# Kernel tuning notes

Hardware: AMD Instinct MI355X
Metric: run time of the kernel (lower is better)

## Reference

```python
import jax, jax.numpy as jnp
import numpy as np

N = 25000      # nodes per type
E = 300000     # weight-edge rows
K = 16         # neighbors
F = 64         # in_feat
A = 64         # atten_dim
DW = 64        # weight_dim
CB = 8         # num_bit_conv
CV = 8         # num_vector_conv
OUT = 64       # out_feat
IN_K = CB * F + CV * (3 + 2 + 1)


def setup_inputs() -> dict:
    key = jax.random.key(0)
    ks = jax.random.split(key, 40)
    s = 0.05
    d = {}
    d['eu'] = jax.random.normal(ks[0], (N, F), jnp.float32)
    d['ei'] = jax.random.normal(ks[1], (N, F), jnp.float32)
    d['et'] = jax.random.normal(ks[2], (N, F), jnp.float32)
    d['ew'] = jax.random.normal(ks[3], (E, DW), jnp.float32)
    names = ['u_iw_j', 'u_tw_j', 'i_uw_j', 'i_tw_j', 't_uw_j', 't_iw_j']
    for i, nm in enumerate(names):
        d[nm] = jax.random.randint(ks[4 + i], (N, K), 0, N, jnp.int64 if jax.config.jax_enable_x64 else jnp.int32)
        d[nm.replace('_j', '_w')] = jax.random.randint(ks[10 + i], (N, K), 0, E, jnp.int64 if jax.config.jax_enable_x64 else jnp.int32)
    # per-type Attention1 params: user, item, tag
    for i, t in enumerate(['user', 'item', 'tag']):
        b = 16 + 4 * i
        d[f'W1_{t}'] = jax.random.normal(ks[b], (F + DW, A), jnp.float32) * s
        d[f'W2_{t}'] = jax.random.normal(ks[b + 1], (F, A), jnp.float32) * s
        d[f'b_{t}'] = jax.random.normal(ks[b + 2], (1, A), jnp.float32) * s
        d[f'v_{t}'] = jax.random.normal(ks[b + 3], (1, A), jnp.float32) * s
    d['U'] = jax.random.normal(ks[28], (F, A), jnp.float32) * s
    d['q'] = jax.random.normal(ks[29], (1, A), jnp.float32) * s
    d['p'] = jax.random.normal(ks[30], (1, A), jnp.float32) * s
    d['W_bit'] = jax.random.normal(ks[31], (CB, 3), jnp.float32) * s       # Conv2d(1,CB,(3,1))
    d['W_vec1'] = jax.random.normal(ks[32], (CV, 1, F), jnp.float32) * s   # Conv2d(1,CV,(1,F))
    d['W_vec2'] = jax.random.normal(ks[33], (CV, 2, F), jnp.float32) * s
    d['W_vec3'] = jax.random.normal(ks[34], (CV, 3, F), jnp.float32) * s
    d['Wf'] = jax.random.normal(ks[35], (IN_K, OUT), jnp.float32) * s
    d['bf'] = jax.random.normal(ks[36], (1, OUT), jnp.float32) * s
    return d


def _atten1(ev, ej, ew, v_j, v_w, W1, W2, b, v):
    ejp = jnp.concatenate([jnp.zeros((1, ej.shape[1]), ej.dtype), ej], axis=0)
    ewp = jnp.concatenate([jnp.zeros((1, ew.shape[1]), ew.dtype), ew], axis=0)
    eNj = ejp[v_j]                                  # [N,K,F]
    eNw = ewp[v_w]                                  # [N,K,DW]
    eNv = jnp.broadcast_to(ev[:, None, :], (ev.shape[0], v_j.shape[1], ev.shape[1]))
    eN_vw = jnp.concatenate([eNv, eNw], axis=-1)    # [N,K,F+DW]
    av = jnp.einsum('nkd,da->nka', eN_vw, W1) + jnp.einsum('nkf,fa->nka', eNj, W2) + b
    x = jax.nn.relu(av) @ v.T                       # [N,K,1]
    a = jax.nn.softmax(x, axis=1)
    return jnp.sum(a * eNj, axis=1)                 # [N,F]


def _atten2(u, i, t, U, q, p):
    uit = jnp.stack([u, i, t], axis=1)              # [N,3,F]
    x = jnp.einsum('nsf,fa->nsa', uit, U) + q
    x = jax.nn.relu(x) @ p.T                        # [N,3,1]
    b = jax.nn.softmax(x, axis=1)
    return b * uit                                  # [N,3,F]


def _conv(eN, W_bit, W_vec1, W_vec2, W_vec3):
    # eN: [N,3,F]
    bit = jax.nn.relu(jnp.einsum('njf,cj->ncf', eN, W_bit))       # [N,CB,F]
    bit = bit.reshape(bit.shape[0], -1)
    vec = []
    for j, W in ((1, W_vec1), (2, W_vec2), (3, W_vec3)):
        win = jnp.stack([eN[:, s:s + j, :] for s in range(3 - j + 1)], axis=1)  # [N,4-j,j,F]
        y = jax.nn.relu(jnp.einsum('nsjf,cjf->ncs', win, W))       # [N,CV,4-j]
        vec.append(y.reshape(y.shape[0], -1))
    return jnp.concatenate([bit] + vec, axis=1)                    # [N,IN_K]


def _forward(eu, ei, et, ew, params, idx):
    (W1u, W2u, bu, vu, W1i, W2i, bi, vi, W1t, W2t, bt, vt,
     U, q, p, W_bit, W_vec1, W_vec2, W_vec3, Wf, bf) = params
    (u_iw_j, u_iw_w, u_tw_j, u_tw_w, i_uw_j, i_uw_w,
     i_tw_j, i_tw_w, t_uw_j, t_uw_w, t_iw_j, t_iw_w) = idx
    eu_iN = _atten1(eu, ei, ew, u_iw_j, u_iw_w, W1i, W2i, bi, vi)
    eu_tN = _atten1(eu, et, ew, u_tw_j, u_tw_w, W1t, W2t, bt, vt)
    ei_uN = _atten1(ei, eu, ew, i_uw_j, i_uw_w, W1u, W2u, bu, vu)
    ei_tN = _atten1(ei, et, ew, i_tw_j, i_tw_w, W1t, W2t, bt, vt)
    et_uN = _atten1(et, eu, ew, t_uw_j, t_uw_w, W1u, W2u, bu, vu)
    et_iN = _atten1(et, ei, ew, t_iw_j, t_iw_w, W1i, W2i, bi, vi)
    euN = _atten2(eu, eu_iN, eu_tN, U, q, p)
    eiN = _atten2(ei_uN, ei, ei_tN, U, q, p)
    etN = _atten2(et_uN, et_iN, et, U, q, p)
    out = []
    for eN in (euN, eiN, etN):
        c = _conv(eN, W_bit, W_vec1, W_vec2, W_vec3)
        out.append(jax.nn.relu(c @ Wf + bf))
    return tuple(out)


def reference(eu, ei, et, ew,
              u_iw_j, u_iw_w, u_tw_j, u_tw_w, i_uw_j, i_uw_w, i_tw_j, i_tw_w,
              t_uw_j, t_uw_w, t_iw_j, t_iw_w,
              W1_user, W2_user, b_user, v_user,
              W1_item, W2_item, b_item, v_item,
              W1_tag, W2_tag, b_tag, v_tag,
              U, q, p, W_bit, W_vec1, W_vec2, W_vec3, Wf, bf):
    params = (W1_user, W2_user, b_user, v_user, W1_item, W2_item, b_item, v_item,
              W1_tag, W2_tag, b_tag, v_tag, U, q, p, W_bit, W_vec1, W_vec2, W_vec3, Wf, bf)
    idx = (u_iw_j, u_iw_w, u_tw_j, u_tw_w, i_uw_j, i_uw_w,
           i_tw_j, i_tw_w, t_uw_j, t_uw_w, t_iw_j, t_iw_w)
    return _forward(eu, ei, et, ew, params, idx)
```

## Files before the change

kernel.cpp:

```cpp
#include <hip/hip_runtime.h>
#include <math.h>

#define NN 25000
#define EE 300000
#define NT 1563
#define NT64 391
#define ET64 4688

typedef __attribute__((ext_vector_type(8))) short bf16x8;
typedef __attribute__((ext_vector_type(4))) float f32x4;
typedef __attribute__((ext_vector_type(2))) float f32x2;
typedef __attribute__((ext_vector_type(2))) __fp16 h2;

__device__ __forceinline__ unsigned short f2bf(float f) {
    union { float f; unsigned u; } a; a.f = f;
    unsigned r = (a.u + 0x7fffu + ((a.u >> 16) & 1u)) >> 16;
    return (unsigned short)r;
}
__device__ __forceinline__ unsigned pack2(float lo, float hi) {
    return (unsigned)f2bf(lo) | ((unsigned)f2bf(hi) << 16);
}
__device__ __forceinline__ float bflo(unsigned p) {
    union { unsigned u; float f; } a; a.u = p << 16; return a.f;
}
__device__ __forceinline__ float bfhi(unsigned p) {
    union { unsigned u; float f; } a; a.u = p & 0xffff0000u; return a.f;
}
__device__ __forceinline__ unsigned packfp8x4(float a, float b, float c, float d) {
    int v = __builtin_amdgcn_cvt_pk_fp8_f32(a, b, 0, 0);
    v = __builtin_amdgcn_cvt_pk_fp8_f32(c, d, v, 1);
    return (unsigned)v;
}
__device__ __forceinline__ unsigned pkh(float lo, float hi) {
    h2 r = __builtin_amdgcn_cvt_pkrtz(lo, hi);
    return __builtin_bit_cast(unsigned, r);
}
template<bool HI>
__device__ __forceinline__ h2 fp8toh(unsigned v) {
#if __has_builtin(__builtin_amdgcn_cvt_scalef32_pk_f16_fp8)
    return __builtin_amdgcn_cvt_scalef32_pk_f16_fp8((int)v, 1.0f, HI);
#else
    f32x2 f = __builtin_amdgcn_cvt_pk_f32_fp8((int)v, HI);
    return __builtin_amdgcn_cvt_pkrtz(f.x, f.y);
#endif
}
__device__ __forceinline__ float hdot(h2 a, h2 b, float c) {
#if __has_builtin(__builtin_amdgcn_fdot2)
    return __builtin_amdgcn_fdot2(a, b, c, false);
#else
    return c + (float)a[0] * (float)b[0] + (float)a[1] * (float)b[1];
#endif
}
__device__ __forceinline__ h2 hmax0(h2 a) {
    h2 z; z[0] = (__fp16)0.f; z[1] = (__fp16)0.f;
#if __has_builtin(__builtin_elementwise_max)
    return __builtin_elementwise_max(a, z);
#else
    h2 r;
    r[0] = a[0] > z[0] ? a[0] : z[0];
    r[1] = a[1] > z[1] ? a[1] : z[1];
    return r;
#endif
}

__global__ __launch_bounds__(256) void head_kernel(
    const float* __restrict__ ew,
    const float* __restrict__ eu, const float* __restrict__ ei, const float* __restrict__ et,
    const float* __restrict__ W1u, const float* __restrict__ W1i, const float* __restrict__ W1t,
    const float* __restrict__ W2u, const float* __restrict__ W2i, const float* __restrict__ W2t,
    const float* __restrict__ bu, const float* __restrict__ bi, const float* __restrict__ bt,
    unsigned char* __restrict__ gw8, unsigned* __restrict__ preB,
    unsigned char* __restrict__ JG)
{
    __shared__ __align__(16) unsigned short stA[64 * 72];
    __shared__ __align__(16) float cS[64 * 68];
    const int t = threadIdx.x;
    const int lane = t & 63, wv = t >> 6;
    const int l15 = lane & 15, quad = lane >> 4;
    const int cw = wv * 16 + l15;
    const int bx = blockIdx.x;

    if (bx < ET64) {
        if (bx == 0 && t < 48) {
            int w = t >> 4;
            ((unsigned*)(gw8 + (size_t)w * (EE + 1) * 64))[t & 15] = 0u;
        }
        const float* Ws[3] = { W1u + 4096, W1i + 4096, W1t + 4096 };
        bf16x8 bf[3][2];
        #pragma unroll
        for (int w = 0; w < 3; ++w)
            #pragma unroll
            for (int ks = 0; ks < 2; ++ks)
                #pragma unroll
                for (int j = 0; j < 8; ++j)
                    bf[w][ks][j] = (short)f2bf(Ws[w][(ks * 32 + quad * 8 + j) * 64 + cw]);

        const int rowBase = bx * 64;
        #pragma unroll
        for (int i = 0; i < 4; ++i) {
            int idx = t + i * 256;
            int row = idx >> 4, cg = idx & 15;
            int gr = rowBase + row;
            float4 v4 = (gr < EE) ? *(const float4*)(ew + (size_t)gr * 64 + cg * 4)
                                  : make_float4(0.f, 0.f, 0.f, 0.f);
            uint2 pk = { pack2(v4.x, v4.y), pack2(v4.z, v4.w) };
            *(uint2*)&stA[row * 72 + cg * 4] = pk;
        }
        __syncthreads();
        bf16x8 af[4][2];
        #pragma unroll
        for (int m = 0; m < 4; ++m)
            #pragma unroll
            for (int ks = 0; ks < 2; ++ks)
                af[m][ks] = *(const bf16x8*)&stA[(m * 16 + l15) * 72 + ks * 32 + quad * 8];

        #pragma unroll
        for (int w = 0; w < 3; ++w) {
            if (w) __syncthreads();
            f32x4 acc[4];
            #pragma unroll
            for (int m = 0; m < 4; ++m) {
                acc[m].x = 0; acc[m].y = 0; acc[m].z = 0; acc[m].w = 0;
                #pragma unroll
                for (int ks = 0; ks < 2; ++ks)
                    acc[m] = __builtin_amdgcn_mfma_f32_16x16x32_bf16(af[m][ks], bf[w][ks], acc[m], 0, 0, 0);
                #pragma unroll
                for (int r = 0; r < 4; ++r)
                    cS[(m * 16 + quad * 4 + r) * 68 + cw] = acc[m][r];
            }
            __syncthreads();
            unsigned char* outg = gw8 + (size_t)w * (EE + 1) * 64 + 64;
            #pragma unroll
            for (int i = 0; i < 2; ++i) {
                int task = t + i * 256;
                int row = task >> 3, seg = task & 7;
                int gr = rowBase + row;
                if (gr < EE) {
                    float4 a = *(const float4*)&cS[row * 68 + seg * 8];
                    float4 b = *(const float4*)&cS[row * 68 + seg * 8 + 4];
                    uint2 pk = { packfp8x4(a.x, a.y, a.z, a.w),
                                 packfp8x4(b.x, b.y, b.z, b.w) };
                    *(uint2*)(outg + (size_t)gr * 64 + seg * 8) = pk;
                }
            }
        }
    } else {
        const int yy = bx - ET64;
        const int y = yy / NT64;
        const int rowBase = (yy - y * NT64) * 64;
        if (rowBase == 0 && t < 48)
            ((unsigned*)(JG + (size_t)y * (NN + 1) * 192))[t] = 0u;
        const float* X; const float* Wa; const float* Wb; const float* W2;
        const float* ba; const float* bb; int oa, ob;
        switch (y) {
            case 0:  X = eu; Wa = W1i; ba = bi; oa = 0; Wb = W1t; bb = bt; ob = 1; W2 = W2u; break;
            case 1:  X = ei; Wa = W1u; ba = bu; oa = 2; Wb = W1t; bb = bt; ob = 3; W2 = W2i; break;
            default: X = et; Wa = W1u; ba = bu; oa = 4; Wb = W1i; bb = bi; ob = 5; W2 = W2t; break;
        }
        const float* Ws[3] = { Wa, Wb, W2 };
        const float bias_cw[3] = { ba[cw], bb[cw], 0.f };
        bf16x8 bf[3][2];
        #pragma unroll
        for (int w = 0; w < 3; ++w)
            #pragma unroll
            for (int ks = 0; ks < 2; ++ks)
                #pragma unroll
                for (int j = 0; j < 8; ++j)
                    bf[w][ks][j] = (short)f2bf(Ws[w][(ks * 32 + quad * 8 + j) * 64 + cw]);

        #pragma unroll
        for (int i = 0; i < 4; ++i) {
            int idx = t + i * 256;
            int row = idx >> 4, cg = idx & 15;
            int gr = rowBase + row;
            float4 v4 = (gr < NN) ? *(const float4*)(X + (size_t)gr * 64 + cg * 4)
                                  : make_float4(0.f, 0.f, 0.f, 0.f);
            uint2 pk = { pack2(v4.x, v4.y), pack2(v4.z, v4.w) };
            *(uint2*)&stA[row * 72 + cg * 4] = pk;
        }
        __syncthreads();
        bf16x8 af[4][2];
        #pragma unroll
        for (int m = 0; m < 4; ++m)
            #pragma unroll
            for (int ks = 0; ks < 2; ++ks)
                af[m][ks] = *(const bf16x8*)&stA[(m * 16 + l15) * 72 + ks * 32 + quad * 8];

        #pragma unroll
        for (int w = 0; w < 3; ++w) {
            if (w) __syncthreads();
            f32x4 acc[4];
            #pragma unroll
            for (int m = 0; m < 4; ++m) {
                acc[m].x = 0; acc[m].y = 0; acc[m].z = 0; acc[m].w = 0;
                #pragma unroll
                for (int ks = 0; ks < 2; ++ks)
                    acc[m] = __builtin_amdgcn_mfma_f32_16x16x32_bf16(af[m][ks], bf[w][ks], acc[m], 0, 0, 0);
                #pragma unroll
                for (int r = 0; r < 4; ++r)
                    cS[(m * 16 + quad * 4 + r) * 68 + cw] = acc[m][r] + bias_cw[w];
            }
            __syncthreads();
            #pragma unroll
            for (int i = 0; i < 2; ++i) {
                int task = t + i * 256;
                int row = task >> 3, seg = task & 7;
                int gr = rowBase + row;
                if (gr >= NN) continue;
                float4 a = *(const float4*)&cS[row * 68 + seg * 8];
                float4 b = *(const float4*)&cS[row * 68 + seg * 8 + 4];
                if (w < 2) {
                    int oi = (w == 0) ? oa : ob;
                    uint4 pk = { pkh(a.x, a.y), pkh(a.z, a.w),
                                 pkh(b.x, b.y), pkh(b.z, b.w) };
                    *(uint4*)(preB + ((size_t)oi * NN + gr) * 32 + seg * 4) = pk;
                } else {
                    unsigned char* dst = JG + ((size_t)y * (NN + 1) + gr + 1) * 192;
                    uint2 gj = { packfp8x4(a.x, a.y, a.z, a.w),
                                 packfp8x4(b.x, b.y, b.z, b.w) };
                    *(uint2*)(dst + seg * 8) = gj;
                    uint4 ej = *(const uint4*)&stA[row * 72 + seg * 8];
                    *(uint4*)(dst + 64 + seg * 16) = ej;
                }
            }
        }
    }
}

__global__ __launch_bounds__(256) void atten1_kernel(
    const unsigned* __restrict__ preB, const unsigned char* __restrict__ gw8,
    const unsigned char* __restrict__ JG,
    const float* __restrict__ vu, const float* __restrict__ vi, const float* __restrict__ vt,
    const int* __restrict__ u_iw_j, const int* __restrict__ u_iw_w,
    const int* __restrict__ u_tw_j, const int* __restrict__ u_tw_w,
    const int* __restrict__ i_uw_j, const int* __restrict__ i_uw_w,
    const int* __restrict__ i_tw_j, const int* __restrict__ i_tw_w,
    const int* __restrict__ t_uw_j, const int* __restrict__ t_uw_w,
    const int* __restrict__ t_iw_j, const int* __restrict__ t_iw_w,
    unsigned* __restrict__ aoB)
{
    const int g = blockIdx.y;
    const int p = blockIdx.x & 1;
    const int tile = blockIdx.x >> 1;
    int y; const int* Vj; const int* Vw;
    switch (g * 2 + p) {
        case 0:  y = 2; Vj = i_uw_j; Vw = i_uw_w; break;
        case 1:  y = 4; Vj = t_uw_j; Vw = t_uw_w; break;
        case 2:  y = 0; Vj = u_iw_j; Vw = u_iw_w; break;
        case 3:  y = 5; Vj = t_iw_j; Vw = t_iw_w; break;
        case 4:  y = 1; Vj = u_tw_j; Vw = u_tw_w; break;
        default: y = 3; Vj = i_tw_j; Vw = i_tw_w; break;
    }
    const float* v = (g == 0) ? vu : (g == 1) ? vi : vt;
    const unsigned* pre = preB + (size_t)y * NN * 32;
    const unsigned char* gw = gw8 + (size_t)g * (EE + 1) * 64;
    const unsigned char* jg = JG + (size_t)g * (NN + 1) * 192;
    unsigned*            out = aoB + (size_t)y * NN * 32;

    const int lane = threadIdx.x & 63;
    const int n = tile * 4 + (threadIdx.x >> 6);
    const int q = lane >> 4, r = lane & 15;

    const uint2 prep = *(const uint2*)(pre + (size_t)n * 32 + 2 * r);
    const h2 pre01 = __builtin_bit_cast(h2, prep.x);
    const h2 pre23 = __builtin_bit_cast(h2, prep.y);
    const float4 v4 = *(const float4*)(v + r * 4);
    const h2 v01h = __builtin_amdgcn_cvt_pkrtz(v4.x, v4.y);
    const h2 v23h = __builtin_amdgcn_cvt_pkrtz(v4.z, v4.w);

    const int4 wi = *(const int4*)(Vw + n * 16 + q * 4);
    const int4 ji = *(const int4*)(Vj + n * 16 + q * 4);
    const int wid[4] = { wi.x, wi.y, wi.z, wi.w };
    const int jid[4] = { ji.x, ji.y, ji.z, ji.w };

    unsigned gwv[4], gjv[4]; uint2 ejv[4];
    #pragma unroll
    for (int i = 0; i < 4; ++i)
        gwv[i] = *(const unsigned*)(gw + (size_t)wid[i] * 64 + r * 4);
    #pragma unroll
    for (int i = 0; i < 4; ++i) {
        const unsigned char* row = jg + (size_t)jid[i] * 192;
        gjv[i] = *(const unsigned*)(row + r * 4);
        ejv[i] = *(const uint2*)(row + 64 + r * 8);
    }

    float xk[4];
    #pragma unroll
    for (int i = 0; i < 4; ++i) {
        h2 g01 = fp8toh<false>(gwv[i]);
        h2 g23 = fp8toh<true>(gwv[i]);
        h2 j01 = fp8toh<false>(gjv[i]);
        h2 j23 = fp8toh<true>(gjv[i]);
        h2 z01 = hmax0(pre01 + g01 + j01);
        h2 z23 = hmax0(pre23 + g23 + j23);
        float x = hdot(z01, v01h, 0.f);
        x = hdot(z23, v23h, x);
        x += __shfl_xor(x, 1, 64);
        x += __shfl_xor(x, 2, 64);
        x += __shfl_xor(x, 4, 64);
        x += __shfl_xor(x, 8, 64);
        xk[i] = x;
    }
    float m = fmaxf(fmaxf(xk[0], xk[1]), fmaxf(xk[2], xk[3]));
    m = fmaxf(m, __shfl_xor(m, 16, 64));
    m = fmaxf(m, __shfl_xor(m, 32, 64));
    float e0 = __expf(xk[0] - m), e1 = __expf(xk[1] - m);
    float e2 = __expf(xk[2] - m), e3 = __expf(xk[3] - m);
    float s = (e0 + e1) + (e2 + e3);
    s += __shfl_xor(s, 16, 64);
    s += __shfl_xor(s, 32, 64);
    const float inv = 1.f / s;

    float a0 = 0.f, a1 = 0.f, a2 = 0.f, a3 = 0.f;
    const float wgt[4] = { e0 * inv, e1 * inv, e2 * inv, e3 * inv };
    #pragma unroll
    for (int i = 0; i < 4; ++i) {
        a0 = fmaf(wgt[i], bflo(ejv[i].x), a0);
        a1 = fmaf(wgt[i], bfhi(ejv[i].x), a1);
        a2 = fmaf(wgt[i], bflo(ejv[i].y), a2);
        a3 = fmaf(wgt[i], bfhi(ejv[i].y), a3);
    }
    a0 += __shfl_xor(a0, 16, 64); a0 += __shfl_xor(a0, 32, 64);
    a1 += __shfl_xor(a1, 16, 64); a1 += __shfl_xor(a1, 32, 64);
    a2 += __shfl_xor(a2, 16, 64); a2 += __shfl_xor(a2, 32, 64);
    a3 += __shfl_xor(a3, 16, 64); a3 += __shfl_xor(a3, 32, 64);
    if (q == 0) {
        uint2 pk = { pack2(a0, a1), pack2(a2, a3) };
        *(uint2*)(out + (size_t)n * 32 + 2 * r) = pk;
    }
}

__global__ __launch_bounds__(256, 3) void tail_kernel(
    const float* __restrict__ eu, const float* __restrict__ ei, const float* __restrict__ et,
    const unsigned* __restrict__ aoB,
    const float* __restrict__ U, const float* __restrict__ q, const float* __restrict__ p,
    const float* __restrict__ Wbit, const float* __restrict__ Wv1,
    const float* __restrict__ Wv2, const float* __restrict__ Wv3,
    const float* __restrict__ Wf, const float* __restrict__ bfv,
    float* __restrict__ out)
{
    __shared__ __align__(16) unsigned short uitA[48 * 72];
    __shared__ __align__(16) unsigned short eNA[48 * 72];
    __shared__ __align__(16) unsigned short wcf[6 * 64 * 8];
    __shared__ __align__(16) unsigned short c_sh[16 * 584];
    __shared__ float G_sh[48 * 52];
    __shared__ float xpart[4 * 48];
    __shared__ float bcoef[16 * 4];

    const int t = threadIdx.x;
    const int lane = t & 63;
    const int wv = t >> 6;
    const int l15 = lane & 15;
    const int quad = lane >> 4;
    const int type = blockIdx.y;
    const float* xf = (type == 0) ? eu : (type == 1) ? ei : et;
    const int cw = wv * 16 + l15;
    const float qv = q[cw], pv = p[cw], bfb = bfv[cw];

    float wb[8][3];
    #pragma unroll
    for (int c = 0; c < 8; ++c)
        #pragma unroll
        for (int s = 0; s < 3; ++s) wb[c][s] = Wbit[c * 3 + s];

    bf16x8 ufrag[2];
    #pragma unroll
    for (int ks = 0; ks < 2; ++ks)
        #pragma unroll
        for (int j = 0; j < 8; ++j) {
            int f = ks * 32 + quad * 8 + j;
            ufrag[ks][j] = (short)f2bf(U[f * 64 + cw]);
        }
    bf16x8 wff[18];
    #pragma unroll
    for (int ks = 0; ks < 18; ++ks)
        #pragma unroll
        for (int j = 0; j < 8; ++j) {
            int k = ks * 32 + quad * 8 + j;
            float w = (k < 560) ? Wf[(size_t)k * 64 + cw] : 0.f;
            wff[ks][j] = (short)f2bf(w);
        }
    for (int slot = t; slot < 384; slot += 256) {
        int fi = slot >> 6, l = slot & 63;
        int nt_ = fi >> 1, ks = fi & 1;
        int r = nt_ * 16 + (l & 15);
        unsigned short vals[8];
        #pragma unroll
        for (int j = 0; j < 8; ++j) {
            int f = ks * 32 + (l >> 4) * 8 + j;
            float wv_;
            if (r < 8)       wv_ = Wv1[r * 64 + f];
            else if (r < 24) { int u = r - 8;  wv_ = Wv2[(u >> 1) * 128 + (u & 1) * 64 + f]; }
            else             { int u = r - 24; wv_ = Wv3[(u / 3) * 192 + (u % 3) * 64 + f]; }
            vals[j] = f2bf(wv_);
        }
        uint4 pk = { (unsigned)vals[0] | ((unsigned)vals[1] << 16),
                     (unsigned)vals[2] | ((unsigned)vals[3] << 16),
                     (unsigned)vals[4] | ((unsigned)vals[5] << 16),
                     (unsigned)vals[6] | ((unsigned)vals[7] << 16) };
        *(uint4*)&wcf[slot * 8] = pk;
    }

    for (int tile = blockIdx.x; tile < NT; tile += gridDim.x) {
        const int nodeBase = tile * 16;
        __syncthreads();
        #pragma unroll
        for (int i = 0; i < 3; ++i) {
            int idx = t + i * 256;
            int row = idx >> 4, cg = idx & 15;
            int nl = row / 3, s = row - nl * 3;
            int n = nodeBase + nl;
            uint2 pk;
            if (s == type) {
                float4 v4 = (n < NN) ? *(const float4*)(xf + (size_t)n * 64 + cg * 4)
                                     : make_float4(0.f, 0.f, 0.f, 0.f);
                pk.x = pack2(v4.x, v4.y); pk.y = pack2(v4.z, v4.w);
            } else {
                int aoidx = (type == 0) ? (s - 1)
                          : (type == 1) ? ((s == 0) ? 2 : 3)
                                        : ((s == 0) ? 4 : 5);
                pk = (n < NN) ? *(const uint2*)(aoB + ((size_t)aoidx * NN + n) * 32 + cg * 2)
                              : make_uint2(0u, 0u);
            }
            *(uint2*)&uitA[row * 72 + cg * 4] = pk;
        }
        __syncthreads();
        {
            f32x4 av[3];
            #pragma unroll
            for (int mt = 0; mt < 3; ++mt) { av[mt].x = 0; av[mt].y = 0; av[mt].z = 0; av[mt].w = 0; }
            #pragma unroll
            for (int mt = 0; mt < 3; ++mt)
                #pragma unroll
                for (int ks = 0; ks < 2; ++ks) {
                    bf16x8 a = *(const bf16x8*)&uitA[(mt * 16 + l15) * 72 + ks * 32 + quad * 8];
                    av[mt] = __builtin_amdgcn_mfma_f32_16x16x32_bf16(a, ufrag[ks], av[mt], 0, 0, 0);
                }
            #pragma unroll
            for (int mt = 0; mt < 3; ++mt)
                #pragma unroll
                for (int r = 0; r < 4; ++r) {
                    float val = fmaxf(av[mt][r] + qv, 0.f) * pv;
                    val += __shfl_xor(val, 1, 64); val += __shfl_xor(val, 2, 64);
                    val += __shfl_xor(val, 4, 64); val += __shfl_xor(val, 8, 64);
                    if (l15 == 0) xpart[wv * 48 + mt * 16 + quad * 4 + r] = val;
                }
        }
        __syncthreads();
        if (t < 16) {
            float xv[3];
            #pragma unroll
            for (int s = 0; s < 3; ++s)
                xv[s] = xpart[t * 3 + s] + xpart[48 + t * 3 + s]
                      + xpart[96 + t * 3 + s] + xpart[144 + t * 3 + s];
            float mm = fmaxf(xv[0], fmaxf(xv[1], xv[2]));
            float e0 = __expf(xv[0] - mm), e1 = __expf(xv[1] - mm), e2 = __expf(xv[2] - mm);
            float inv = 1.f / (e0 + e1 + e2);
            bcoef[t * 4 + 0] = e0 * inv; bcoef[t * 4 + 1] = e1 * inv; bcoef[t * 4 + 2] = e2 * inv;
        }
        __syncthreads();
        #pragma unroll
        for (int i = 0; i < 2; ++i) {
            int task = t + i * 256;
            int nl = task >> 5, fp = task & 31;
            float b0 = bcoef[nl * 4], b1 = bcoef[nl * 4 + 1], b2 = bcoef[nl * 4 + 2];
            unsigned u0 = *(const unsigned*)&uitA[(nl * 3 + 0) * 72 + fp * 2];
            unsigned u1 = *(const unsigned*)&uitA[(nl * 3 + 1) * 72 + fp * 2];
            unsigned u2 = *(const unsigned*)&uitA[(nl * 3 + 2) * 72 + fp * 2];
            float e0l = b0 * bflo(u0), e0h = b0 * bfhi(u0);
            float e1l = b1 * bflo(u1), e1h = b1 * bfhi(u1);
            float e2l = b2 * bflo(u2), e2h = b2 * bfhi(u2);
            *(unsigned*)&eNA[(nl * 3 + 0) * 72 + fp * 2] = pack2(e0l, e0h);
            *(unsigned*)&eNA[(nl * 3 + 1) * 72 + fp * 2] = pack2(e1l, e1h);
            *(unsigned*)&eNA[(nl * 3 + 2) * 72 + fp * 2] = pack2(e2l, e2h);
            #pragma unroll
            for (int c = 0; c < 8; ++c) {
                float lo = fmaxf(wb[c][0] * e0l + wb[c][1] * e1l + wb[c][2] * e2l, 0.f);
                float hi = fmaxf(wb[c][0] * e0h + wb[c][1] * e1h + wb[c][2] * e2h, 0.f);
                *(unsigned*)&c_sh[nl * 584 + c * 64 + fp * 2] = pack2(lo, hi);
            }
        }
        __syncthreads();
        #pragma unroll
        for (int pi = 0; pi < 3; ++pi) {
            int pr = wv + pi * 4;
            if (pr < 9) {
                int mm = pr / 3, nn_ = pr - mm * 3;
                f32x4 g; g.x = 0; g.y = 0; g.z = 0; g.w = 0;
                #pragma unroll
                for (int ks = 0; ks < 2; ++ks) {
                    bf16x8 a = *(const bf16x8*)&eNA[(mm * 16 + l15) * 72 + ks * 32 + quad * 8];
                    bf16x8 b = *(const bf16x8*)&wcf[((nn_ * 2 + ks) * 64 + lane) * 8];
                    g = __builtin_amdgcn_mfma_f32_16x16x32_bf16(a, b, g, 0, 0, 0);
                }
                #pragma unroll
                for (int r = 0; r < 4; ++r)
                    G_sh[(mm * 16 + quad * 4 + r) * 52 + nn_ * 16 + l15] = g[r];
            }
        }
        __syncthreads();
        #pragma unroll
        for (int i = 0; i < 4; ++i) {
            int task = t + i * 256;
            int vvv = task >> 4, nl = task & 15;
            unsigned short res = 0;
            if (vvv < 24) {
                int c = vvv / 3, s = vvv - c * 3;
                res = f2bf(fmaxf(G_sh[(nl * 3 + s) * 52 + c], 0.f));
            } else if (vvv < 40) {
                int u = vvv - 24, c = u >> 1, s = u & 1;
                float val = G_sh[(nl * 3 + s) * 52 + 8 + 2 * c]
                          + G_sh[(nl * 3 + s + 1) * 52 + 8 + 2 * c + 1];
                res = f2bf(fmaxf(val, 0.f));
            } else if (vvv < 48) {
                int c = vvv - 40;
                float val = G_sh[(nl * 3 + 0) * 52 + 24 + 3 * c]
                          + G_sh[(nl * 3 + 1) * 52 + 24 + 3 * c + 1]
                          + G_sh[(nl * 3 + 2) * 52 + 24 + 3 * c + 2];
                res = f2bf(fmaxf(val, 0.f));
            }
            c_sh[nl * 584 + 512 + vvv] = res;
        }
        __syncthreads();
        {
            f32x4 acc; acc.x = 0; acc.y = 0; acc.z = 0; acc.w = 0;
            const unsigned short* ap = &c_sh[l15 * 584 + quad * 8];
            #pragma unroll
            for (int ks = 0; ks < 18; ++ks) {
                bf16x8 a = *(const bf16x8*)(ap + ks * 32);
                acc = __builtin_amdgcn_mfma_f32_16x16x32_bf16(a, wff[ks], acc, 0, 0, 0);
            }
            float* outT = out + (size_t)type * NN * 64;
            #pragma unroll
            for (int r = 0; r < 4; ++r) {
                int node = nodeBase + quad * 4 + r;
                if (node < NN) outT[(size_t)node * 64 + cw] = fmaxf(acc[r] + bfb, 0.f);
            }
        }
    }
}

extern "C" void kernel_launch(void* const* d_in, const int* in_sizes, int n_in,
                              void* d_out, int out_size, void* d_ws, size_t ws_size,
                              hipStream_t stream)
{
    const float* eu = (const float*)d_in[0];
    const float* ei = (const float*)d_in[1];
    const float* et = (const float*)d_in[2];
    const float* ew = (const float*)d_in[3];
    const int* u_iw_j = (const int*)d_in[4];
    const int* u_iw_w = (const int*)d_in[5];
    const int* u_tw_j = (const int*)d_in[6];
    const int* u_tw_w = (const int*)d_in[7];
    const int* i_uw_j = (const int*)d_in[8];
    const int* i_uw_w = (const int*)d_in[9];
    const int* i_tw_j = (const int*)d_in[10];
    const int* i_tw_w = (const int*)d_in[11];
    const int* t_uw_j = (const int*)d_in[12];
    const int* t_uw_w = (const int*)d_in[13];
    const int* t_iw_j = (const int*)d_in[14];
    const int* t_iw_w = (const int*)d_in[15];
    const float* W1_user = (const float*)d_in[16];
    const float* W2_user = (const float*)d_in[17];
    const float* b_user  = (const float*)d_in[18];
    const float* v_user  = (const float*)d_in[19];
    const float* W1_item = (const float*)d_in[20];
    const float* W2_item = (const float*)d_in[21];
    const float* b_item  = (const float*)d_in[22];
    const float* v_item  = (const float*)d_in[23];
    const float* W1_tag  = (const float*)d_in[24];
    const float* W2_tag  = (const float*)d_in[25];
    const float* b_tag   = (const float*)d_in[26];
    const float* v_tag   = (const float*)d_in[27];
    const float* U    = (const float*)d_in[28];
    const float* q    = (const float*)d_in[29];
    const float* p    = (const float*)d_in[30];
    const float* Wbit = (const float*)d_in[31];
    const float* Wv1  = (const float*)d_in[32];
    const float* Wv2  = (const float*)d_in[33];
    const float* Wv3  = (const float*)d_in[34];
    const float* Wf   = (const float*)d_in[35];
    const float* bfv  = (const float*)d_in[36];
    float* out = (float*)d_out;

    unsigned char* gw8 = (unsigned char*)d_ws;
    unsigned* preB = (unsigned*)(gw8 + (size_t)3 * (EE + 1) * 64);
    unsigned char* JG = (unsigned char*)(preB + (size_t)6 * NN * 32);
    unsigned* aoB = (unsigned*)(JG + (size_t)3 * (NN + 1) * 192);

    const dim3 blk(256);

    head_kernel<<<ET64 + 3 * NT64, blk, 0, stream>>>(
        ew, eu, ei, et,
        W1_user, W1_item, W1_tag, W2_user, W2_item, W2_tag,
        b_user, b_item, b_tag, gw8, preB, JG);

    atten1_kernel<<<dim3(2 * (NN / 4), 3), blk, 0, stream>>>(
        preB, gw8, JG, v_user, v_item, v_tag,
        u_iw_j, u_iw_w, u_tw_j, u_tw_w, i_uw_j, i_uw_w,
        i_tw_j, i_tw_w, t_uw_j, t_uw_w, t_iw_j, t_iw_w, aoB);

    tail_kernel<<<dim3(256, 3), blk, 0, stream>>>(
        eu, ei, et, aoB,
        U, q, p, Wbit, Wv1, Wv2, Wv3, Wf, bfv, out);
}
```

Before: 396.0 us.

## Software-pipeline atten1 gathers across five nodes per wave with fewer blocks

Each wave in atten1_kernel now handles five nodes, strided 5000 apart, instead of one. The grid shrinks from 12500x3 to 2500x3 blocks. Index loads, gather loads and embedding loads are staged two and one iterations ahead, so dependent global gathers overlap with the softmax and aggregation compute of the current node. The weighted sum also uses packed f32x2 FMAs. The cost is many more live registers, which can lower occupancy, and fewer blocks to hide latency across the GPU.

```diff
diff --git a/kernel.cpp b/kernel.cpp
--- a/kernel.cpp
+++ b/kernel.cpp
@@ -241,7 +241,6 @@
 {
     const int g = blockIdx.y;
     const int p = blockIdx.x & 1;
-    const int tile = blockIdx.x >> 1;
     int y; const int* Vj; const int* Vw;
     switch (g * 2 + p) {
         case 0:  y = 2; Vj = i_uw_j; Vw = i_uw_w; break;
@@ -258,76 +257,107 @@
     unsigned*            out = aoB + (size_t)y * NN * 32;
 
     const int lane = threadIdx.x & 63;
-    const int n = tile * 4 + (threadIdx.x >> 6);
     const int q = lane >> 4, r = lane & 15;
-
-    const uint2 prep = *(const uint2*)(pre + (size_t)n * 32 + 2 * r);
-    const h2 pre01 = __builtin_bit_cast(h2, prep.x);
-    const h2 pre23 = __builtin_bit_cast(h2, prep.y);
+    const int n0 = (blockIdx.x >> 1) * 4 + (threadIdx.x >> 6);
+
     const float4 v4 = *(const float4*)(v + r * 4);
     const h2 v01h = __builtin_amdgcn_cvt_pkrtz(v4.x, v4.y);
     const h2 v23h = __builtin_amdgcn_cvt_pkrtz(v4.z, v4.w);
 
-    const int4 wi = *(const int4*)(Vw + n * 16 + q * 4);
-    const int4 ji = *(const int4*)(Vj + n * 16 + q * 4);
-    const int wid[4] = { wi.x, wi.y, wi.z, wi.w };
-    const int jid[4] = { ji.x, ji.y, ji.z, ji.w };
-
-    unsigned gwv[4], gjv[4]; uint2 ejv[4];
+    int4 wi[5], ji[5];
+    uint2 prep[5];
+    unsigned gwv[5][4], gjv[5][4];
+    uint2 ejv[5][4];
+
+    #define A_STAGE(IT) {                                                     \
+        int nn = n0 + (IT) * 5000;                                            \
+        wi[IT] = *(const int4*)(Vw + (size_t)nn * 16 + q * 4);                \
+        ji[IT] = *(const int4*)(Vj + (size_t)nn * 16 + q * 4);                \
+    }
+    #define B_STAGE(IT) {                                                     \
+        int nn = n0 + (IT) * 5000;                                            \
+        prep[IT] = *(const uint2*)(pre + (size_t)nn * 32 + 2 * r);            \
+        gwv[IT][0] = *(const unsigned*)(gw + (size_t)wi[IT].x * 64 + r * 4);  \
+        gwv[IT][1] = *(const unsigned*)(gw + (size_t)wi[IT].y * 64 + r * 4);  \
+        gwv[IT][2] = *(const unsigned*)(gw + (size_t)wi[IT].z * 64 + r * 4);  \
+        gwv[IT][3] = *(const unsigned*)(gw + (size_t)wi[IT].w * 64 + r * 4);  \
+        gjv[IT][0] = *(const unsigned*)(jg + (size_t)ji[IT].x * 192 + r * 4); \
+        gjv[IT][1] = *(const unsigned*)(jg + (size_t)ji[IT].y * 192 + r * 4); \
+        gjv[IT][2] = *(const unsigned*)(jg + (size_t)ji[IT].z * 192 + r * 4); \
+        gjv[IT][3] = *(const unsigned*)(jg + (size_t)ji[IT].w * 192 + r * 4); \
+    }
+    #define E_STAGE(IT) {                                                     \
+        ejv[IT][0] = *(const uint2*)(jg + (size_t)ji[IT].x * 192 + 64 + r * 8); \
+        ejv[IT][1] = *(const uint2*)(jg + (size_t)ji[IT].y * 192 + 64 + r * 8); \
+        ejv[IT][2] = *(const uint2*)(jg + (size_t)ji[IT].z * 192 + 64 + r * 8); \
+        ejv[IT][3] = *(const uint2*)(jg + (size_t)ji[IT].w * 192 + 64 + r * 8); \
+    }
+
+    A_STAGE(0);
+    A_STAGE(1);
+    B_STAGE(0);
+
     #pragma unroll
-    for (int i = 0; i < 4; ++i)
-        gwv[i] = *(const unsigned*)(gw + (size_t)wid[i] * 64 + r * 4);
-    #pragma unroll
-    for (int i = 0; i < 4; ++i) {
-        const unsigned char* row = jg + (size_t)jid[i] * 192;
-        gjv[i] = *(const unsigned*)(row + r * 4);
-        ejv[i] = *(const uint2*)(row + 64 + r * 8);
-    }
-
-    float xk[4];
-    #pragma unroll
-    for (int i = 0; i < 4; ++i) {
-        h2 g01 = fp8toh<false>(gwv[i]);
-        h2 g23 = fp8toh<true>(gwv[i]);
-        h2 j01 = fp8toh<false>(gjv[i]);
-        h2 j23 = fp8toh<true>(gjv[i]);
-        h2 z01 = hmax0(pre01 + g01 + j01);
-        h2 z23 = hmax0(pre23 + g23 + j23);
-        float x = hdot(z01, v01h, 0.f);
-        x = hdot(z23, v23h, x);
-        x += __shfl_xor(x, 1, 64);
-        x += __shfl_xor(x, 2, 64);
-        x += __shfl_xor(x, 4, 64);
-        x += __shfl_xor(x, 8, 64);
-        xk[i] = x;
-    }
-    float m = fmaxf(fmaxf(xk[0], xk[1]), fmaxf(xk[2], xk[3]));
-    m = fmaxf(m, __shfl_xor(m, 16, 64));
-    m = fmaxf(m, __shfl_xor(m, 32, 64));
-    float e0 = __expf(xk[0] - m), e1 = __expf(xk[1] - m);
-    float e2 = __expf(xk[2] - m), e3 = __expf(xk[3] - m);
-    float s = (e0 + e1) + (e2 + e3);
-    s += __shfl_xor(s, 16, 64);
-    s += __shfl_xor(s, 32, 64);
-    const float inv = 1.f / s;
-
-    float a0 = 0.f, a1 = 0.f, a2 = 0.f, a3 = 0.f;
-    const float wgt[4] = { e0 * inv, e1 * inv, e2 * inv, e3 * inv };
-    #pragma unroll
-    for (int i = 0; i < 4; ++i) {
-        a0 = fmaf(wgt[i], bflo(ejv[i].x), a0);
-        a1 = fmaf(wgt[i], bfhi(ejv[i].x), a1);
-        a2 = fmaf(wgt[i], bflo(ejv[i].y), a2);
-        a3 = fmaf(wgt[i], bfhi(ejv[i].y), a3);
-    }
-    a0 += __shfl_xor(a0, 16, 64); a0 += __shfl_xor(a0, 32, 64);
-    a1 += __shfl_xor(a1, 16, 64); a1 += __shfl_xor(a1, 32, 64);
-    a2 += __shfl_xor(a2, 16, 64); a2 += __shfl_xor(a2, 32, 64);
-    a3 += __shfl_xor(a3, 16, 64); a3 += __shfl_xor(a3, 32, 64);
-    if (q == 0) {
-        uint2 pk = { pack2(a0, a1), pack2(a2, a3) };
-        *(uint2*)(out + (size_t)n * 32 + 2 * r) = pk;
-    }
+    for (int it = 0; it < 5; ++it) {
+        E_STAGE(it);
+        if (it + 1 < 5) B_STAGE(it + 1);
+        if (it + 2 < 5) A_STAGE(it + 2);
+
+        const h2 pre01 = __builtin_bit_cast(h2, prep[it].x);
+        const h2 pre23 = __builtin_bit_cast(h2, prep[it].y);
+
+        float xk[4];
+        #pragma unroll
+        for (int i = 0; i < 4; ++i) {
+            h2 g01 = fp8toh<false>(gwv[it][i]);
+            h2 g23 = fp8toh<true>(gwv[it][i]);
+            h2 j01 = fp8toh<false>(gjv[it][i]);
+            h2 j23 = fp8toh<true>(gjv[it][i]);
+            h2 z01 = hmax0(pre01 + g01 + j01);
+            h2 z23 = hmax0(pre23 + g23 + j23);
+            float x = hdot(z01, v01h, 0.f);
+            x = hdot(z23, v23h, x);
+            x += __shfl_xor(x, 1, 64);
+            x += __shfl_xor(x, 2, 64);
+            x += __shfl_xor(x, 4, 64);
+            x += __shfl_xor(x, 8, 64);
+            xk[i] = x;
+        }
+        float m = fmaxf(fmaxf(xk[0], xk[1]), fmaxf(xk[2], xk[3]));
+        m = fmaxf(m, __shfl_xor(m, 16, 64));
+        m = fmaxf(m, __shfl_xor(m, 32, 64));
+        float e0 = __expf(xk[0] - m), e1 = __expf(xk[1] - m);
+        float e2 = __expf(xk[2] - m), e3 = __expf(xk[3] - m);
+        float s = (e0 + e1) + (e2 + e3);
+        s += __shfl_xor(s, 16, 64);
+        s += __shfl_xor(s, 32, 64);
+        const float inv = 1.f / s;
+
+        const float wgt[4] = { e0 * inv, e1 * inv, e2 * inv, e3 * inv };
+        f32x2 A01; A01.x = 0.f; A01.y = 0.f;
+        f32x2 A23; A23.x = 0.f; A23.y = 0.f;
+        #pragma unroll
+        for (int i = 0; i < 4; ++i) {
+            f32x2 w2; w2.x = wgt[i]; w2.y = wgt[i];
+            f32x2 e01; e01.x = bflo(ejv[it][i].x); e01.y = bfhi(ejv[it][i].x);
+            f32x2 e23; e23.x = bflo(ejv[it][i].y); e23.y = bfhi(ejv[it][i].y);
+            A01 = e01 * w2 + A01;
+            A23 = e23 * w2 + A23;
+        }
+        float a0 = A01.x, a1 = A01.y, a2 = A23.x, a3 = A23.y;
+        a0 += __shfl_xor(a0, 16, 64); a0 += __shfl_xor(a0, 32, 64);
+        a1 += __shfl_xor(a1, 16, 64); a1 += __shfl_xor(a1, 32, 64);
+        a2 += __shfl_xor(a2, 16, 64); a2 += __shfl_xor(a2, 32, 64);
+        a3 += __shfl_xor(a3, 16, 64); a3 += __shfl_xor(a3, 32, 64);
+        if (q == 0) {
+            int nn = n0 + it * 5000;
+            uint2 pk = { pack2(a0, a1), pack2(a2, a3) };
+            *(uint2*)(out + (size_t)nn * 32 + 2 * r) = pk;
+        }
+    }
+    #undef A_STAGE
+    #undef B_STAGE
+    #undef E_STAGE
 }
 
 __global__ __launch_bounds__(256, 3) void tail_kernel(
@@ -595,7 +625,7 @@
         W1_user, W1_item, W1_tag, W2_user, W2_item, W2_tag,
         b_user, b_item, b_tag, gw8, preB, JG);
 
-    atten1_kernel<<<dim3(2 * (NN / 4), 3), blk, 0, stream>>>(
+    atten1_kernel<<<dim3(2500, 3), blk, 0, stream>>>(
         preB, gw8, JG, v_user, v_item, v_tag,
         u_iw_j, u_iw_w, u_tw_j, u_tw_w, i_uw_j, i_uw_w,
         i_tw_j, i_tw_w, t_uw_j, t_uw_w, t_iw_j, t_iw_w, aoB);
```

After: 399.2 us. No clear change (+0.8%).

## Process two row tiles per head block and double-buffer the LDS output staging

Applied to the files above, without the earlier changes.

Each head_kernel block now handles 128 rows as two 64-row tiles. This halves the block count and amortises the per-block conversion of the weight fragments to bf16. All three weight GEMMs are issued back-to-back into separate accumulators, and the results are staged through two alternating LDS buffers so that fewer barriers sit between the MFMA and store phases. The atten1 weighted-sum loop is also rewritten with packed float2 FMAs. The costs are higher register pressure (12 accumulators), more LDS per block and reduced grid parallelism.

```diff
diff --git a/kernel.cpp b/kernel.cpp
--- a/kernel.cpp
+++ b/kernel.cpp
@@ -4,8 +4,8 @@
 #define NN 25000
 #define EE 300000
 #define NT 1563
-#define NT64 391
-#define ET64 4688
+#define ET128 2344
+#define NT128 196
 
 typedef __attribute__((ext_vector_type(8))) short bf16x8;
 typedef __attribute__((ext_vector_type(4))) float f32x4;
@@ -73,14 +73,15 @@
     unsigned char* __restrict__ JG)
 {
     __shared__ __align__(16) unsigned short stA[64 * 72];
-    __shared__ __align__(16) float cS[64 * 68];
+    __shared__ __align__(16) float cSa[64 * 68];
+    __shared__ __align__(16) float cSb[64 * 68];
     const int t = threadIdx.x;
     const int lane = t & 63, wv = t >> 6;
     const int l15 = lane & 15, quad = lane >> 4;
     const int cw = wv * 16 + l15;
     const int bx = blockIdx.x;
 
-    if (bx < ET64) {
+    if (bx < ET128) {
         if (bx == 0 && t < 48) {
             int w = t >> 4;
             ((unsigned*)(gw8 + (size_t)w * (EE + 1) * 64))[t & 15] = 0u;
@@ -95,60 +96,78 @@
                 for (int j = 0; j < 8; ++j)
                     bf[w][ks][j] = (short)f2bf(Ws[w][(ks * 32 + quad * 8 + j) * 64 + cw]);
 
-        const int rowBase = bx * 64;
-        #pragma unroll
-        for (int i = 0; i < 4; ++i) {
-            int idx = t + i * 256;
-            int row = idx >> 4, cg = idx & 15;
-            int gr = rowBase + row;
-            float4 v4 = (gr < EE) ? *(const float4*)(ew + (size_t)gr * 64 + cg * 4)
-                                  : make_float4(0.f, 0.f, 0.f, 0.f);
-            uint2 pk = { pack2(v4.x, v4.y), pack2(v4.z, v4.w) };
-            *(uint2*)&stA[row * 72 + cg * 4] = pk;
-        }
-        __syncthreads();
-        bf16x8 af[4][2];
-        #pragma unroll
-        for (int m = 0; m < 4; ++m)
-            #pragma unroll
-            for (int ks = 0; ks < 2; ++ks)
-                af[m][ks] = *(const bf16x8*)&stA[(m * 16 + l15) * 72 + ks * 32 + quad * 8];
-
-        #pragma unroll
-        for (int w = 0; w < 3; ++w) {
-            if (w) __syncthreads();
-            f32x4 acc[4];
-            #pragma unroll
-            for (int m = 0; m < 4; ++m) {
-                acc[m].x = 0; acc[m].y = 0; acc[m].z = 0; acc[m].w = 0;
+        #pragma unroll
+        for (int tile = 0; tile < 2; ++tile) {
+            const int rowBase = bx * 128 + tile * 64;
+            #pragma unroll
+            for (int i = 0; i < 4; ++i) {
+                int idx = t + i * 256;
+                int row = idx >> 4, cg = idx & 15;
+                int gr = rowBase + row;
+                float4 v4 = (gr < EE) ? *(const float4*)(ew + (size_t)gr * 64 + cg * 4)
+                                      : make_float4(0.f, 0.f, 0.f, 0.f);
+                uint2 pk = { pack2(v4.x, v4.y), pack2(v4.z, v4.w) };
+                *(uint2*)&stA[row * 72 + cg * 4] = pk;
+            }
+            __syncthreads();
+            bf16x8 af[4][2];
+            #pragma unroll
+            for (int m = 0; m < 4; ++m)
                 #pragma unroll
                 for (int ks = 0; ks < 2; ++ks)
-                    acc[m] = __builtin_amdgcn_mfma_f32_16x16x32_bf16(af[m][ks], bf[w][ks], acc[m], 0, 0, 0);
-                #pragma unroll
-                for (int r = 0; r < 4; ++r)
-                    cS[(m * 16 + quad * 4 + r) * 68 + cw] = acc[m][r];
-            }
-            __syncthreads();
-            unsigned char* outg = gw8 + (size_t)w * (EE + 1) * 64 + 64;
-            #pragma unroll
-            for (int i = 0; i < 2; ++i) {
-                int task = t + i * 256;
-                int row = task >> 3, seg = task & 7;
-                int gr = rowBase + row;
-                if (gr < EE) {
-                    float4 a = *(const float4*)&cS[row * 68 + seg * 8];
-                    float4 b = *(const float4*)&cS[row * 68 + seg * 8 + 4];
-                    uint2 pk = { packfp8x4(a.x, a.y, a.z, a.w),
-                                 packfp8x4(b.x, b.y, b.z, b.w) };
-                    *(uint2*)(outg + (size_t)gr * 64 + seg * 8) = pk;
+                    af[m][ks] = *(const bf16x8*)&stA[(m * 16 + l15) * 72 + ks * 32 + quad * 8];
+
+            f32x4 acc[3][4];
+            #pragma unroll
+            for (int w = 0; w < 3; ++w)
+                #pragma unroll
+                for (int m = 0; m < 4; ++m) {
+                    acc[w][m].x = 0; acc[w][m].y = 0; acc[w][m].z = 0; acc[w][m].w = 0;
+                    #pragma unroll
+                    for (int ks = 0; ks < 2; ++ks)
+                        acc[w][m] = __builtin_amdgcn_mfma_f32_16x16x32_bf16(af[m][ks], bf[w][ks], acc[w][m], 0, 0, 0);
                 }
-            }
+
+            #define EG_WRITE(BUF, W) {                                               \
+                _Pragma("unroll")                                                    \
+                for (int m = 0; m < 4; ++m)                                          \
+                    _Pragma("unroll")                                                \
+                    for (int r = 0; r < 4; ++r)                                      \
+                        BUF[(m * 16 + quad * 4 + r) * 68 + cw] = acc[W][m][r];       \
+            }
+            #define EG_STORE(BUF, W) {                                               \
+                unsigned char* outg = gw8 + (size_t)(W) * (EE + 1) * 64 + 64;        \
+                _Pragma("unroll")                                                    \
+                for (int i = 0; i < 2; ++i) {                                        \
+                    int task = t + i * 256;                                          \
+                    int row = task >> 3, seg = task & 7;                             \
+                    int gr = rowBase + row;                                          \
+                    if (gr < EE) {                                                   \
+                        float4 a = *(const float4*)&BUF[row * 68 + seg * 8];         \
+                        float4 b = *(const float4*)&BUF[row * 68 + seg * 8 + 4];     \
+                        uint2 pk = { packfp8x4(a.x, a.y, a.z, a.w),                  \
+                                     packfp8x4(b.x, b.y, b.z, b.w) };                \
+                        *(uint2*)(outg + (size_t)gr * 64 + seg * 8) = pk;            \
+                    }                                                                \
+                }                                                                    \
+            }
+            EG_WRITE(cSa, 0);
+            __syncthreads();
+            EG_STORE(cSa, 0);
+            EG_WRITE(cSb, 1);
+            __syncthreads();
+            EG_STORE(cSb, 1);
+            EG_WRITE(cSa, 2);
+            __syncthreads();
+            EG_STORE(cSa, 2);
+            #undef EG_WRITE
+            #undef EG_STORE
         }
     } else {
-        const int yy = bx - ET64;
-        const int y = yy / NT64;
-        const int rowBase = (yy - y * NT64) * 64;
-        if (rowBase == 0 && t < 48)
+        const int yy = bx - ET128;
+        const int y = yy / NT128;
+        const int rowBase0 = (yy - y * NT128) * 128;
+        if (rowBase0 == 0 && t < 48)
             ((unsigned*)(JG + (size_t)y * (NN + 1) * 192))[t] = 0u;
         const float* X; const float* Wa; const float* Wb; const float* W2;
         const float* ba; const float* bb; int oa, ob;
@@ -169,60 +188,81 @@
                     bf[w][ks][j] = (short)f2bf(Ws[w][(ks * 32 + quad * 8 + j) * 64 + cw]);
 
         #pragma unroll
-        for (int i = 0; i < 4; ++i) {
-            int idx = t + i * 256;
-            int row = idx >> 4, cg = idx & 15;
-            int gr = rowBase + row;
-            float4 v4 = (gr < NN) ? *(const float4*)(X + (size_t)gr * 64 + cg * 4)
-                                  : make_float4(0.f, 0.f, 0.f, 0.f);
-            uint2 pk = { pack2(v4.x, v4.y), pack2(v4.z, v4.w) };
-            *(uint2*)&stA[row * 72 + cg * 4] = pk;
-        }
-        __syncthreads();
-        bf16x8 af[4][2];
-        #pragma unroll
-        for (int m = 0; m < 4; ++m)
-            #pragma unroll
-            for (int ks = 0; ks < 2; ++ks)
-                af[m][ks] = *(const bf16x8*)&stA[(m * 16 + l15) * 72 + ks * 32 + quad * 8];
-
-        #pragma unroll
-        for (int w = 0; w < 3; ++w) {
-            if (w) __syncthreads();
-            f32x4 acc[4];
-            #pragma unroll
-            for (int m = 0; m < 4; ++m) {
-                acc[m].x = 0; acc[m].y = 0; acc[m].z = 0; acc[m].w = 0;
+        for (int tile = 0; tile < 2; ++tile) {
+            const int rowBase = rowBase0 + tile * 64;
+            if (tile) __syncthreads();
+            #pragma unroll
+            for (int i = 0; i < 4; ++i) {
+                int idx = t + i * 256;
+                int row = idx >> 4, cg = idx & 15;
+                int gr = rowBase + row;
+                float4 v4 = (gr < NN) ? *(const float4*)(X + (size_t)gr * 64 + cg * 4)
+                                      : make_float4(0.f, 0.f, 0.f, 0.f);
+                uint2 pk = { pack2(v4.x, v4.y), pack2(v4.z, v4.w) };
+                *(uint2*)&stA[row * 72 + cg * 4] = pk;
+            }
+            __syncthreads();
+            bf16x8 af[4][2];
+            #pragma unroll
+            for (int m = 0; m < 4; ++m)
                 #pragma unroll
                 for (int ks = 0; ks < 2; ++ks)
-                    acc[m] = __builtin_amdgcn_mfma_f32_16x16x32_bf16(af[m][ks], bf[w][ks], acc[m], 0, 0, 0);
-                #pragma unroll
-                for (int r = 0; r < 4; ++r)
-                    cS[(m * 16 + quad * 4 + r) * 68 + cw] = acc[m][r] + bias_cw[w];
-            }
-            __syncthreads();
-            #pragma unroll
-            for (int i = 0; i < 2; ++i) {
-                int task = t + i * 256;
-                int row = task >> 3, seg = task & 7;
-                int gr = rowBase + row;
-                if (gr >= NN) continue;
-                float4 a = *(const float4*)&cS[row * 68 + seg * 8];
-                float4 b = *(const float4*)&cS[row * 68 + seg * 8 + 4];
-                if (w < 2) {
-                    int oi = (w == 0) ? oa : ob;
-                    uint4 pk = { pkh(a.x, a.y), pkh(a.z, a.w),
-                                 pkh(b.x, b.y), pkh(b.z, b.w) };
-                    *(uint4*)(preB + ((size_t)oi * NN + gr) * 32 + seg * 4) = pk;
-                } else {
-                    unsigned char* dst = JG + ((size_t)y * (NN + 1) + gr + 1) * 192;
-                    uint2 gj = { packfp8x4(a.x, a.y, a.z, a.w),
-                                 packfp8x4(b.x, b.y, b.z, b.w) };
-                    *(uint2*)(dst + seg * 8) = gj;
-                    uint4 ej = *(const uint4*)&stA[row * 72 + seg * 8];
-                    *(uint4*)(dst + 64 + seg * 16) = ej;
+                    af[m][ks] = *(const bf16x8*)&stA[(m * 16 + l15) * 72 + ks * 32 + quad * 8];
+
+            f32x4 acc[3][4];
+            #pragma unroll
+            for (int w = 0; w < 3; ++w)
+                #pragma unroll
+                for (int m = 0; m < 4; ++m) {
+                    acc[w][m].x = 0; acc[w][m].y = 0; acc[w][m].z = 0; acc[w][m].w = 0;
+                    #pragma unroll
+                    for (int ks = 0; ks < 2; ++ks)
+                        acc[w][m] = __builtin_amdgcn_mfma_f32_16x16x32_bf16(af[m][ks], bf[w][ks], acc[w][m], 0, 0, 0);
                 }
-            }
+
+            #define NG_WRITE(BUF, W) {                                                     \
+                _Pragma("unroll")                                                          \
+                for (int m = 0; m < 4; ++m)                                                \
+                    _Pragma("unroll")                                                      \
+                    for (int r = 0; r < 4; ++r)                                            \
+                        BUF[(m * 16 + quad * 4 + r) * 68 + cw] = acc[W][m][r] + bias_cw[W];\
+            }
+            #define NG_STORE(BUF, W) {                                                     \
+                _Pragma("unroll")                                                          \
+                for (int i = 0; i < 2; ++i) {                                              \
+                    int task = t + i * 256;                                                \
+                    int row = task >> 3, seg = task & 7;                                   \
+                    int gr = rowBase + row;                                                \
+                    if (gr < NN) {                                                         \
+                        float4 a = *(const float4*)&BUF[row * 68 + seg * 8];               \
+                        float4 b = *(const float4*)&BUF[row * 68 + seg * 8 + 4];           \
+                        if ((W) < 2) {                                                     \
+                            int oi = ((W) == 0) ? oa : ob;                                 \
+                            uint4 pk = { pkh(a.x, a.y), pkh(a.z, a.w),                     \
+                                         pkh(b.x, b.y), pkh(b.z, b.w) };                   \
+                            *(uint4*)(preB + ((size_t)oi * NN + gr) * 32 + seg * 4) = pk;  \
+                        } else {                                                           \
+                            unsigned char* dst = JG + ((size_t)y * (NN + 1) + gr + 1) * 192;\
+                            uint2 gj = { packfp8x4(a.x, a.y, a.z, a.w),                    \
+                                         packfp8x4(b.x, b.y, b.z, b.w) };                  \
+                            *(uint2*)(dst + seg * 8) = gj;                                 \
+                            uint4 ej = *(const uint4*)&stA[row * 72 + seg * 8];            \
+                            *(uint4*)(dst + 64 + seg * 16) = ej;                           \
+                        }                                                                  \
+                    }                                                                      \
+                }                                                                          \
+            }
+            NG_WRITE(cSa, 0);
+            __syncthreads();
+            NG_STORE(cSa, 0);
+            NG_WRITE(cSb, 1);
+            __syncthreads();
+            NG_STORE(cSb, 1);
+            NG_WRITE(cSa, 2);
+            __syncthreads();
+            NG_STORE(cSa, 2);
+            #undef NG_WRITE
+            #undef NG_STORE
         }
     }
 }
@@ -311,15 +351,18 @@
     s += __shfl_xor(s, 32, 64);
     const float inv = 1.f / s;
 
-    float a0 = 0.f, a1 = 0.f, a2 = 0.f, a3 = 0.f;
     const float wgt[4] = { e0 * inv, e1 * inv, e2 * inv, e3 * inv };
+    f32x2 A01; A01.x = 0.f; A01.y = 0.f;
+    f32x2 A23; A23.x = 0.f; A23.y = 0.f;
     #pragma unroll
     for (int i = 0; i < 4; ++i) {
-        a0 = fmaf(wgt[i], bflo(ejv[i].x), a0);
-        a1 = fmaf(wgt[i], bfhi(ejv[i].x), a1);
-        a2 = fmaf(wgt[i], bflo(ejv[i].y), a2);
-        a3 = fmaf(wgt[i], bfhi(ejv[i].y), a3);
-    }
+        f32x2 w2; w2.x = wgt[i]; w2.y = wgt[i];
+        f32x2 e01; e01.x = bflo(ejv[i].x); e01.y = bfhi(ejv[i].x);
+        f32x2 e23; e23.x = bflo(ejv[i].y); e23.y = bfhi(ejv[i].y);
+        A01 = e01 * w2 + A01;
+        A23 = e23 * w2 + A23;
+    }
+    float a0 = A01.x, a1 = A01.y, a2 = A23.x, a3 = A23.y;
     a0 += __shfl_xor(a0, 16, 64); a0 += __shfl_xor(a0, 32, 64);
     a1 += __shfl_xor(a1, 16, 64); a1 += __shfl_xor(a1, 32, 64);
     a2 += __shfl_xor(a2, 16, 64); a2 += __shfl_xor(a2, 32, 64);
@@ -590,7 +633,7 @@
 
     const dim3 blk(256);
 
-    head_kernel<<<ET64 + 3 * NT64, blk, 0, stream>>>(
+    head_kernel<<<ET128 + 3 * NT128, blk, 0, stream>>>(
         ew, eu, ei, et,
         W1_user, W1_item, W1_tag, W2_user, W2_item, W2_tag,
         b_user, b_item, b_tag, gw8, preB, JG);
```

Measured after the change: 390.3 us, median of 2. No clear change (-1.4%).
